# Kernel tuning notes

Hardware: AMD Instinct MI355X
Metric: run time of the kernel (lower is better)

Reference implementation:

```python
import jax, jax.numpy as jnp
import numpy as np

B, N, T, F = 8, 5000, 24, 10
H = 128
HEADS = 4
HORIZON = 6
E = 80000
NEG_SLOPE = 0.2


def setup_inputs() -> dict:
    key = jax.random.key(0)
    ks = jax.random.split(key, 24)
    s = 0.1
    inp = {
        'x': jax.random.normal(ks[0], (B, N, T, F), jnp.float32),
        'w_ih0': jax.random.normal(ks[1], (3 * H, F), jnp.float32) * s,
        'w_hh0': jax.random.normal(ks[2], (3 * H, H), jnp.float32) * s,
        'b_ih0': jax.random.normal(ks[3], (3 * H,), jnp.float32) * s,
        'b_hh0': jax.random.normal(ks[4], (3 * H,), jnp.float32) * s,
        'w_ih1': jax.random.normal(ks[5], (3 * H, H), jnp.float32) * s,
        'w_hh1': jax.random.normal(ks[6], (3 * H, H), jnp.float32) * s,
        'b_ih1': jax.random.normal(ks[7], (3 * H,), jnp.float32) * s,
        'b_hh1': jax.random.normal(ks[8], (3 * H,), jnp.float32) * s,
        'gat1_w': jax.random.normal(ks[9], (HEADS * H, H), jnp.float32) * s,
        'gat1_asrc': jax.random.normal(ks[10], (HEADS, H), jnp.float32) * s,
        'gat1_adst': jax.random.normal(ks[11], (HEADS, H), jnp.float32) * s,
        'gat1_b': jax.random.normal(ks[12], (H,), jnp.float32) * s,
        'gat2_w': jax.random.normal(ks[13], (HEADS * H, H), jnp.float32) * s,
        'gat2_asrc': jax.random.normal(ks[14], (HEADS, H), jnp.float32) * s,
        'gat2_adst': jax.random.normal(ks[15], (HEADS, H), jnp.float32) * s,
        'gat2_b': jax.random.normal(ks[16], (H,), jnp.float32) * s,
        'fc_w': jax.random.normal(ks[17], (HORIZON, H), jnp.float32) * s,
        'fc_b': jax.random.normal(ks[18], (HORIZON,), jnp.float32) * s,
        'edge_index': jax.random.randint(ks[19], (2, E), 0, N, jnp.int64),
    }
    return inp


def _gru_layer(xs, w_ih, w_hh, b_ih, b_hh):
    # xs: [BN, T, Fin] -> outputs [BN, T, H] (PyTorch GRU gate order r,z,n)
    gi = jnp.einsum('btf,gf->btg', xs, w_ih) + b_ih  # [BN, T, 3H]
    h0 = jnp.zeros((xs.shape[0], H), xs.dtype)

    def step(h, gi_t):
        gh = h @ w_hh.T + b_hh
        i_r, i_z, i_n = jnp.split(gi_t, 3, axis=-1)
        h_r, h_z, h_n = jnp.split(gh, 3, axis=-1)
        r = jax.nn.sigmoid(i_r + h_r)
        z = jax.nn.sigmoid(i_z + h_z)
        n = jnp.tanh(i_n + r * h_n)
        h_new = (1.0 - z) * n + z * h
        return h_new, h_new

    _, hs = jax.lax.scan(step, h0, jnp.swapaxes(gi, 0, 1))
    return jnp.swapaxes(hs, 0, 1)


def _gat(h, src, dst, W, a_src, a_dst, b, num_nodes):
    # PyG GATConv, heads=4, concat=False (mean), self-loops already in src/dst
    wh = (h @ W.T).reshape(num_nodes, HEADS, H)          # [BN, heads, H]
    alpha_s = jnp.sum(wh * a_src[None], axis=-1)          # [BN, heads]
    alpha_d = jnp.sum(wh * a_dst[None], axis=-1)
    e = jax.nn.leaky_relu(alpha_s[src] + alpha_d[dst], NEG_SLOPE)  # [Eb, heads]
    emax = jax.ops.segment_max(e, dst, num_segments=num_nodes)
    emax = jnp.where(jnp.isfinite(emax), emax, 0.0)
    ex = jnp.exp(e - emax[dst])
    denom = jax.ops.segment_sum(ex, dst, num_segments=num_nodes)
    alpha = ex / (denom[dst] + 1e-16)                     # segment softmax over incoming edges
    out = jax.ops.segment_sum(alpha[..., None] * wh[src], dst, num_segments=num_nodes)
    return out.mean(axis=1) + b


def _batched_edges(edge_index):
    offsets = (jnp.arange(B, dtype=edge_index.dtype) * N)[:, None]
    src = (edge_index[0][None, :] + offsets).reshape(-1)
    dst = (edge_index[1][None, :] + offsets).reshape(-1)
    loops = jnp.arange(B * N, dtype=edge_index.dtype)     # PyG add_self_loops=True
    return jnp.concatenate([src, loops]), jnp.concatenate([dst, loops])


def reference(x, w_ih0, w_hh0, b_ih0, b_hh0, w_ih1, w_hh1, b_ih1, b_hh1,
              gat1_w, gat1_asrc, gat1_adst, gat1_b,
              gat2_w, gat2_asrc, gat2_adst, gat2_b,
              fc_w, fc_b, edge_index):
    src, dst = _batched_edges(edge_index)
    xs = x.reshape(B * N, T, F)
    h1 = _gru_layer(xs, w_ih0, w_hh0, b_ih0, b_hh0)
    h2 = _gru_layer(h1, w_ih1, w_hh1, b_ih1, b_hh1)
    temporal = h2[:, -1, :]                               # [B*N, H]
    s = jax.nn.relu(_gat(temporal, src, dst, gat1_w, gat1_asrc, gat1_adst, gat1_b, B * N))
    s = jax.nn.relu(_gat(s, src, dst, gat2_w, gat2_asrc, gat2_adst, gat2_b, B * N))
    out = s @ fc_w.T + fc_b
    return out.reshape(B, N, HORIZON)
```

## Files before the change

### kernel.cpp

```cpp
#include <hip/hip_runtime.h>
#include <math.h>

#define T_STEPS 24
#define F_IN 10
#define HDIM 128
#define E_EDGES 80000
#define B_BATCH 8
#define N_NODES 5000
#define BN_TOTAL 40000
#define BE 640000
#define NE 680000

typedef __attribute__((ext_vector_type(8))) short s16x8;
typedef __attribute__((ext_vector_type(4))) short s16x4;
typedef __attribute__((ext_vector_type(4))) float fx4;
typedef __attribute__((ext_vector_type(2))) float fx2;
typedef __attribute__((ext_vector_type(4))) unsigned int ux4;
typedef __attribute__((ext_vector_type(2))) unsigned int ux2;

__device__ __forceinline__ float sigmoidf_(float v) { return 1.f / (1.f + __expf(-v)); }
__device__ __forceinline__ float tanhf_(float v) { float e = __expf(2.f * v); return 1.f - 2.f / (e + 1.f); }

__device__ __forceinline__ short f2b(float f) {
    unsigned u = __float_as_uint(f);
    unsigned r = (u + 0x7fffu + ((u >> 16) & 1u)) >> 16;
    return (short)r;
}
__device__ __forceinline__ unsigned int pkbf(float a, float b) {
    unsigned int r;
    asm("v_cvt_pk_bf16_f32 %0, %1, %2" : "=v"(r) : "v"(a), "v"(b));
    return r;
}

#define VMW0 asm volatile("s_waitcnt vmcnt(0)" ::: "memory")

__global__ void pack_w(const float* __restrict__ wih0, const float* __restrict__ whh0,
                       const float* __restrict__ wih1, const float* __restrict__ whh1,
                       const float* __restrict__ g1w, const float* __restrict__ g2w,
                       short* __restrict__ pk) {
    int id = blockIdx.x * 256 + threadIdx.x;
    if (id >= 290816) return;
    if (id < 147456) {
        int mat = id / 49152, r = id % 49152;
        int nf = r / 2048, r2 = r % 2048, kf = r2 / 512, r3 = r2 % 512, lane = r3 / 8, j = r3 % 8;
        int n = nf * 16 + (lane & 15), k = kf * 32 + (lane >> 4) * 8 + j;
        const float* src = (mat == 0) ? whh0 : (mat == 1) ? whh1 : wih1;
        pk[id] = f2b(src[n * 128 + k]);
    } else if (id < 159744) {
        int r = id - 147456;
        int nf = r / 512, r2 = r % 512, lane = r2 / 8, j = r2 % 8;
        int n = nf * 16 + (lane & 15), k = (lane >> 4) * 8 + j;
        pk[id] = (k < F_IN) ? f2b(wih0[n * F_IN + k]) : (short)0;
    } else {
        const float* src = (id < 225280) ? g1w : g2w;
        int r = (id < 225280) ? (id - 159744) : (id - 225280);
        int nf = r / 2048, r2 = r % 2048, kf = r2 / 512, r3 = r2 % 512, lane = r3 / 8, j = r3 % 8;
        int n = nf * 16 + (lane & 15), k = kf * 32 + (lane >> 4) * 8 + j;
        pk[id] = f2b(src[n * 128 + k]);
    }
}

__global__ __launch_bounds__(512, 1) void gru_mfma(
    const float* __restrict__ x, const short* __restrict__ pk,
    const float* __restrict__ bih0, const float* __restrict__ bhh0,
    const float* __restrict__ bih1, const float* __restrict__ bhh1,
    float* __restrict__ temporal) {
    __shared__ __align__(16) short h1b[64 * 128];
    __shared__ __align__(16) short h2b[64 * 128];
    __shared__ __align__(16) short ih1s[49152];
    __shared__ __align__(16) short ih0s[12288];
    __shared__ __align__(16) float blds[2][4][128];
    const int tid = threadIdx.x;
    const int w = tid >> 6, l = tid & 63;
    const int lm = l & 15, lk = l >> 4;
    const int jb = w * 16 + lk * 4;
    const long sb = (long)blockIdx.x * 64;

    {
        const char* src1 = (const char*)(pk + 98304);
#pragma unroll
        for (int r = 0; r < 12; ++r) {
            const int off = (w * 12 + r) * 1024;
            __builtin_amdgcn_global_load_lds(
                (const __attribute__((address_space(1))) unsigned int*)(src1 + off + l * 16),
                (__attribute__((address_space(3))) unsigned int*)((char*)ih1s + off), 16, 0, 0);
        }
        const char* src0 = (const char*)(pk + 147456);
#pragma unroll
        for (int r = 0; r < 3; ++r) {
            const int off = (w * 3 + r) * 1024;
            __builtin_amdgcn_global_load_lds(
                (const __attribute__((address_space(1))) unsigned int*)(src0 + off + l * 16),
                (__attribute__((address_space(3))) unsigned int*)((char*)ih0s + off), 16, 0, 0);
        }
    }
    if (tid < 128) {
        const int j = tid;
        blds[0][0][j] = bih0[j] + bhh0[j];
        blds[0][1][j] = bih0[128 + j] + bhh0[128 + j];
        blds[0][2][j] = bhh0[256 + j];
        blds[0][3][j] = bih0[256 + j];
    } else if (tid < 256) {
        const int j = tid - 128;
        blds[1][0][j] = bih1[j] + bhh1[j];
        blds[1][1][j] = bih1[128 + j] + bhh1[128 + j];
        blds[1][2][j] = bhh1[256 + j];
        blds[1][3][j] = bih1[256 + j];
    }
    for (int i = tid; i < 64 * 128; i += 512) { h1b[i] = 0; h2b[i] = 0; }

    s16x8 whh0r[3][4], whh1r[3][4];
#pragma unroll
    for (int g = 0; g < 3; ++g)
#pragma unroll
        for (int kf = 0; kf < 4; ++kf) {
            const int idx = ((((g * 8 + w) * 4) + kf) * 64 + l) * 8;
            whh0r[g][kf] = *(const s16x8*)&pk[idx];
            whh1r[g][kf] = *(const s16x8*)&pk[49152 + idx];
        }

    fx4 h1s[4], h2s[4];
#pragma unroll
    for (int mf = 0; mf < 4; ++mf) { h1s[mf] = (fx4)(0.f); h2s[mf] = (fx4)(0.f); }

    VMW0;
    __syncthreads();

    for (int tt = 0; tt < T_STEPS; ++tt) {
        ux4 xu[4];
#pragma unroll
        for (int mf = 0; mf < 4; ++mf) {
            fx2 a0 = (fx2)(0.f), a1 = (fx2)(0.f), a2 = (fx2)(0.f), a3 = (fx2)(0.f);
            const float* xr = x + (sb + mf * 16 + lm) * (T_STEPS * F_IN) + tt * F_IN;
            if (lk == 0) {
                a0 = *(const fx2*)(xr);     a1 = *(const fx2*)(xr + 2);
                a2 = *(const fx2*)(xr + 4); a3 = *(const fx2*)(xr + 6);
            } else if (lk == 1) {
                a0 = *(const fx2*)(xr + 8);
            }
            ux4 t = { pkbf(a0.x, a0.y), pkbf(a1.x, a1.y), pkbf(a2.x, a2.y), pkbf(a3.x, a3.y) };
            xu[mf] = t;
        }
        fx4 acc[4][4];
#pragma unroll
        for (int p = 0; p < 4; ++p) {
            const fx4 bv = *(const fx4*)&blds[0][p][jb];
#pragma unroll
            for (int mf = 0; mf < 4; ++mf) acc[p][mf] = bv;
        }
#pragma unroll
        for (int kf = 0; kf < 4; ++kf) {
            s16x8 bfr[4];
#pragma unroll
            for (int mf = 0; mf < 4; ++mf) {
                const int m = mf * 16 + lm;
                const int slot = (kf * 4 + lk) ^ (m & 7);
                bfr[mf] = *(const s16x8*)&h1b[m * 128 + slot * 8];
            }
#pragma unroll
            for (int g = 0; g < 3; ++g) {
                const int part = (g == 2) ? 2 : g;
#pragma unroll
                for (int mf = 0; mf < 4; ++mf)
                    acc[part][mf] = __builtin_amdgcn_mfma_f32_16x16x32_bf16(whh0r[g][kf], bfr[mf], acc[part][mf], 0, 0, 0);
            }
        }
#pragma unroll
        for (int g = 0; g < 3; ++g) {
            const int part = (g == 2) ? 3 : g;
            const s16x8 af = *(const s16x8*)&ih0s[((g * 8 + w) * 64 + l) * 8];
#pragma unroll
            for (int mf = 0; mf < 4; ++mf)
                acc[part][mf] = __builtin_amdgcn_mfma_f32_16x16x32_bf16(af, __builtin_bit_cast(s16x8, xu[mf]), acc[part][mf], 0, 0, 0);
        }
        ux2 w1[4];
#pragma unroll
        for (int mf = 0; mf < 4; ++mf) {
#pragma unroll
            for (int rg = 0; rg < 4; ++rg) {
                const float r = sigmoidf_(acc[0][mf][rg]);
                const float z = sigmoidf_(acc[1][mf][rg]);
                const float n = tanhf_(acc[3][mf][rg] + r * acc[2][mf][rg]);
                h1s[mf][rg] = (1.f - z) * n + z * h1s[mf][rg];
            }
            ux2 q = { pkbf(h1s[mf][0], h1s[mf][1]), pkbf(h1s[mf][2], h1s[mf][3]) };
            w1[mf] = q;
        }
#pragma unroll
        for (int p = 0; p < 4; ++p) {
            const fx4 bv = *(const fx4*)&blds[1][p][jb];
#pragma unroll
            for (int mf = 0; mf < 4; ++mf) acc[p][mf] = bv;
        }
#pragma unroll
        for (int kf = 0; kf < 4; ++kf) {
            s16x8 bfr[4];
#pragma unroll
            for (int mf = 0; mf < 4; ++mf) {
                const int m = mf * 16 + lm;
                const int slot = (kf * 4 + lk) ^ (m & 7);
                bfr[mf] = *(const s16x8*)&h2b[m * 128 + slot * 8];
            }
#pragma unroll
            for (int g = 0; g < 3; ++g) {
                const int part = (g == 2) ? 2 : g;
#pragma unroll
                for (int mf = 0; mf < 4; ++mf)
                    acc[part][mf] = __builtin_amdgcn_mfma_f32_16x16x32_bf16(whh1r[g][kf], bfr[mf], acc[part][mf], 0, 0, 0);
            }
        }
        __syncthreads();
#pragma unroll
        for (int mf = 0; mf < 4; ++mf) {
            const int m = mf * 16 + lm;
            const int slot = (jb >> 3) ^ (m & 7);
            *(ux2*)&h1b[m * 128 + slot * 8 + (jb & 7)] = w1[mf];
        }
        __syncthreads();
#pragma unroll
        for (int kf = 0; kf < 4; ++kf) {
            s16x8 bfr[4];
#pragma unroll
            for (int mf = 0; mf < 4; ++mf) {
                const int m = mf * 16 + lm;
                const int slot = (kf * 4 + lk) ^ (m & 7);
                bfr[mf] = *(const s16x8*)&h1b[m * 128 + slot * 8];
            }
#pragma unroll
            for (int g = 0; g < 3; ++g) {
                const int part = (g == 2) ? 3 : g;
                const s16x8 af = *(const s16x8*)&ih1s[((((g * 8 + w) * 4) + kf) * 64 + l) * 8];
#pragma unroll
                for (int mf = 0; mf < 4; ++mf)
                    acc[part][mf] = __builtin_amdgcn_mfma_f32_16x16x32_bf16(af, bfr[mf], acc[part][mf], 0, 0, 0);
            }
        }
#pragma unroll
        for (int mf = 0; mf < 4; ++mf) {
#pragma unroll
            for (int rg = 0; rg < 4; ++rg) {
                const float r = sigmoidf_(acc[0][mf][rg]);
                const float z = sigmoidf_(acc[1][mf][rg]);
                const float n = tanhf_(acc[3][mf][rg] + r * acc[2][mf][rg]);
                h2s[mf][rg] = (1.f - z) * n + z * h2s[mf][rg];
            }
            const int m = mf * 16 + lm;
            const int slot = (jb >> 3) ^ (m & 7);
            ux2 q = { pkbf(h2s[mf][0], h2s[mf][1]), pkbf(h2s[mf][2], h2s[mf][3]) };
            *(ux2*)&h2b[m * 128 + slot * 8 + (jb & 7)] = q;
        }
        __syncthreads();
    }
#pragma unroll
    for (int mf = 0; mf < 4; ++mf) {
        const long m = sb + mf * 16 + lm;
        *(fx4*)&temporal[m * 128 + jb] = h2s[mf];
    }
}

__global__ void csr_count(const int* __restrict__ edge1, int* __restrict__ cnt) {
    int e = blockIdx.x * 256 + threadIdx.x;
    if (e >= NE) return;
    int d;
    if (e < BE) { int b = e / E_EDGES; d = edge1[e - b * E_EDGES] + b * N_NODES; }
    else d = e - BE;
    atomicAdd(&cnt[d], 1);
}

__global__ void csr_scan(const int* cnt, int* offs, int* curs) {
    __shared__ int part[1024];
    const int t = threadIdx.x;
    const int base = t * 40;
    int end = base + 40; if (end > BN_TOTAL) end = BN_TOTAL;
    int s = 0;
    for (int i = base; i < end; ++i) s += cnt[i];
    part[t] = s;
    __syncthreads();
    for (int off = 1; off < 1024; off <<= 1) {
        int v = (t >= off) ? part[t - off] : 0;
        __syncthreads();
        part[t] += v;
        __syncthreads();
    }
    int run = part[t] - s;
    for (int i = base; i < end; ++i) {
        int c = cnt[i];
        offs[i] = run; curs[i] = run; run += c;
    }
    if (t == 1023) offs[BN_TOTAL] = NE;
}

__global__ void csr_fill(const int* __restrict__ edge1, int* __restrict__ curs, int* __restrict__ esort) {
    int e = blockIdx.x * 256 + threadIdx.x;
    if (e >= NE) return;
    int d;
    if (e < BE) { int b = e / E_EDGES; d = edge1[e - b * E_EDGES] + b * N_NODES; }
    else d = e - BE;
    int pos = atomicAdd(&curs[d], 1);
    esort[pos] = e;
}

__global__ __launch_bounds__(256, 2) void gat_gemm(const float* __restrict__ feat,
                                                   const short* __restrict__ pkg,
                                                   const float* __restrict__ asrc,
                                                   const float* __restrict__ adst,
                                                   float* __restrict__ wh,
                                                   float* __restrict__ AS, float* __restrict__ AD) {
    __shared__ __align__(16) short fb[128 * 128];
    __shared__ float reda[4][128];
    __shared__ float redb[4][128];
    const int tid = threadIdx.x;
    const int w = tid >> 6, l = tid & 63;
    const int lm = l & 15, lk = l >> 4;
    const int i0 = blockIdx.x * 128;
    const int j0 = blockIdx.y * 128;
#pragma unroll
    for (int it = 0; it < 16; ++it) {
        const int idx = it * 256 + tid;
        const int r = idx >> 5, kq = idx & 31;
        fx4 v = (fx4)(0.f);
        const int row = i0 + r;
        if (row < BN_TOTAL) v = *(const fx4*)&feat[(size_t)row * 128 + kq * 4];
        const int slot = (kq >> 1) ^ (r & 7);
        ux2 pv = { pkbf(v.x, v.y), pkbf(v.z, v.w) };
        *(ux2*)&fb[r * 128 + slot * 8 + (kq & 1) * 4] = pv;
    }
    __syncthreads();
    fx4 acc[2][8];
#pragma unroll
    for (int jf = 0; jf < 2; ++jf)
#pragma unroll
        for (int mf = 0; mf < 8; ++mf) acc[jf][mf] = (fx4)(0.f);
#pragma unroll
    for (int kf = 0; kf < 4; ++kf) {
        s16x8 bfr[8];
#pragma unroll
        for (int mf = 0; mf < 8; ++mf) {
            const int m = mf * 16 + lm;
            const int slot = (kf * 4 + lk) ^ (m & 7);
            bfr[mf] = *(const s16x8*)&fb[m * 128 + slot * 8];
        }
#pragma unroll
        for (int jf = 0; jf < 2; ++jf) {
            const int nf = (j0 >> 4) + w * 2 + jf;
            const s16x8 af = *(const s16x8*)&pkg[((nf * 4 + kf) * 64 + l) * 8];
#pragma unroll
            for (int mf = 0; mf < 8; ++mf)
                acc[jf][mf] = __builtin_amdgcn_mfma_f32_16x16x32_bf16(af, bfr[mf], acc[jf][mf], 0, 0, 0);
        }
    }
    float ps[8], pd[8];
#pragma unroll
    for (int mf = 0; mf < 8; ++mf) { ps[mf] = 0.f; pd[mf] = 0.f; }
#pragma unroll
    for (int jf = 0; jf < 2; ++jf) {
        const int cb = w * 32 + jf * 16 + lk * 4;
        const fx4 s4 = *(const fx4*)&asrc[j0 + cb];
        const fx4 d4 = *(const fx4*)&adst[j0 + cb];
        const int nb = j0 + cb;
#pragma unroll
        for (int mf = 0; mf < 8; ++mf) {
            const int m = i0 + mf * 16 + lm;
            const fx4 a = acc[jf][mf];
            if (m < BN_TOTAL) *(fx4*)&wh[(size_t)m * 512 + nb] = a;
            ps[mf] += a.x * s4.x + a.y * s4.y + a.z * s4.z + a.w * s4.w;
            pd[mf] += a.x * d4.x + a.y * d4.y + a.z * d4.z + a.w * d4.w;
        }
    }
#pragma unroll
    for (int off = 16; off <= 32; off <<= 1) {
#pragma unroll
        for (int mf = 0; mf < 8; ++mf) {
            ps[mf] += __shfl_xor(ps[mf], off);
            pd[mf] += __shfl_xor(pd[mf], off);
        }
    }
    if (lk == 0) {
#pragma unroll
        for (int mf = 0; mf < 8; ++mf) {
            reda[w][mf * 16 + lm] = ps[mf];
            redb[w][mf * 16 + lm] = pd[mf];
        }
    }
    __syncthreads();
    if (tid < 128) {
        const int row = i0 + tid;
        if (row < BN_TOTAL) {
            const float a = reda[0][tid] + reda[1][tid] + reda[2][tid] + reda[3][tid];
            const float b = redb[0][tid] + redb[1][tid] + redb[2][tid] + redb[3][tid];
            AS[row * 4 + (j0 >> 7)] = a;
            AD[row * 4 + (j0 >> 7)] = b;
        }
    }
}

__device__ __forceinline__ int decode_src(int eid, const int* __restrict__ edge0) {
    if (eid < BE) { int b = eid / E_EDGES; return edge0[eid - b * E_EDGES] + b * N_NODES; }
    return eid - BE;
}

__global__ __launch_bounds__(256) void gat_aggregate(const float* __restrict__ wh,
                                                     const float* __restrict__ AS, const float* __restrict__ AD,
                                                     const int* __restrict__ offs, const int* __restrict__ esort,
                                                     const int* __restrict__ edge0, const float* __restrict__ bias,
                                                     float* __restrict__ outf,
                                                     const float* __restrict__ fcw, const float* __restrict__ fcb,
                                                     float* __restrict__ out6) {
    const int lane = threadIdx.x & 63;
    const int bid = blockIdx.x;
    const int d = (bid & 7) * N_NODES + (bid >> 3) * 4 + (threadIdx.x >> 6);
    const int e0 = offs[d], e1 = offs[d + 1];
    const fx4 ad4 = *(const fx4*)&AD[d * 4];
    float mx0 = -1e30f, mx1 = -1e30f, mx2 = -1e30f, mx3 = -1e30f;
    float den0 = 0.f, den1 = 0.f, den2 = 0.f, den3 = 0.f;
    float acc[8] = {0.f, 0.f, 0.f, 0.f, 0.f, 0.f, 0.f, 0.f};
    for (int e = e0; e < e1; ++e) {
        const int src = decode_src(esort[e], edge0);
        const fx4 as4 = *(const fx4*)&AS[src * 4];
        float v0 = as4.x + ad4.x; v0 = v0 > 0.f ? v0 : 0.2f * v0;
        float v1 = as4.y + ad4.y; v1 = v1 > 0.f ? v1 : 0.2f * v1;
        float v2 = as4.z + ad4.z; v2 = v2 > 0.f ? v2 : 0.2f * v2;
        float v3 = as4.w + ad4.w; v3 = v3 > 0.f ? v3 : 0.2f * v3;
        const float n0 = fmaxf(mx0, v0), n1 = fmaxf(mx1, v1), n2 = fmaxf(mx2, v2), n3 = fmaxf(mx3, v3);
        const float c0 = __expf(mx0 - n0), c1 = __expf(mx1 - n1), c2 = __expf(mx2 - n2), c3 = __expf(mx3 - n3);
        const float ex0 = __expf(v0 - n0), ex1 = __expf(v1 - n1), ex2 = __expf(v2 - n2), ex3 = __expf(v3 - n3);
        mx0 = n0; mx1 = n1; mx2 = n2; mx3 = n3;
        den0 = den0 * c0 + ex0; den1 = den1 * c1 + ex1;
        den2 = den2 * c2 + ex2; den3 = den3 * c3 + ex3;
        const float* wr = wh + (size_t)src * 512;
        acc[0] = acc[0] * c0 + ex0 * wr[lane];        acc[1] = acc[1] * c0 + ex0 * wr[64 + lane];
        acc[2] = acc[2] * c1 + ex1 * wr[128 + lane];  acc[3] = acc[3] * c1 + ex1 * wr[192 + lane];
        acc[4] = acc[4] * c2 + ex2 * wr[256 + lane];  acc[5] = acc[5] * c2 + ex2 * wr[320 + lane];
        acc[6] = acc[6] * c3 + ex3 * wr[384 + lane];  acc[7] = acc[7] * c3 + ex3 * wr[448 + lane];
    }
    den0 += 1e-16f; den1 += 1e-16f; den2 += 1e-16f; den3 += 1e-16f;
    const float o0r = 0.25f * (acc[0] / den0 + acc[2] / den1 + acc[4] / den2 + acc[6] / den3) + bias[lane];
    const float o1r = 0.25f * (acc[1] / den0 + acc[3] / den1 + acc[5] / den2 + acc[7] / den3) + bias[64 + lane];
    const float o0 = fmaxf(o0r, 0.f);
    const float o1 = fmaxf(o1r, 0.f);
    if (fcw == nullptr) {
        outf[(size_t)d * 128 + lane] = o0;
        outf[(size_t)d * 128 + 64 + lane] = o1;
    } else {
        float p[6];
#pragma unroll
        for (int m = 0; m < 6; ++m) p[m] = o0 * fcw[m * 128 + lane] + o1 * fcw[m * 128 + 64 + lane];
#pragma unroll
        for (int off = 32; off > 0; off >>= 1) {
#pragma unroll
            for (int m = 0; m < 6; ++m) p[m] += __shfl_down(p[m], off);
        }
        if (lane == 0) {
#pragma unroll
            for (int m = 0; m < 6; ++m) out6[(size_t)d * 6 + m] = p[m] + fcb[m];
        }
    }
}

extern "C" void kernel_launch(void* const* d_in, const int* in_sizes, int n_in,
                              void* d_out, int out_size, void* d_ws, size_t ws_size,
                              hipStream_t stream) {
    const float* x = (const float*)d_in[0];
    const float* wih0 = (const float*)d_in[1];
    const float* whh0 = (const float*)d_in[2];
    const float* bih0 = (const float*)d_in[3];
    const float* bhh0 = (const float*)d_in[4];
    const float* wih1 = (const float*)d_in[5];
    const float* whh1 = (const float*)d_in[6];
    const float* bih1 = (const float*)d_in[7];
    const float* bhh1 = (const float*)d_in[8];
    const float* g1w = (const float*)d_in[9];
    const float* g1as = (const float*)d_in[10];
    const float* g1ad = (const float*)d_in[11];
    const float* g1b = (const float*)d_in[12];
    const float* g2w = (const float*)d_in[13];
    const float* g2as = (const float*)d_in[14];
    const float* g2ad = (const float*)d_in[15];
    const float* g2b = (const float*)d_in[16];
    const float* fcw = (const float*)d_in[17];
    const float* fcb = (const float*)d_in[18];
    const int* eidx = (const int*)d_in[19];
    const int* edge0 = eidx;
    const int* edge1 = eidx + E_EDGES;

    char* ws = (char*)d_ws;
    float* H0 = (float*)ws;
    float* H1 = (float*)(ws + 20480000);
    float* WH = (float*)(ws + 40960000);
    float* AS = (float*)(ws + 122880000);
    float* AD = (float*)(ws + 123520000);
    short* PK = (short*)(ws + 124160000);
    int* OFFS = (int*)(ws + 124765184);
    int* CURS = (int*)(ws + 124925248);
    int* ESORT = (int*)(ws + 125085248);

    hipMemsetAsync(CURS, 0, BN_TOTAL * sizeof(int), stream);
    pack_w<<<1136, 256, 0, stream>>>(wih0, whh0, wih1, whh1, g1w, g2w, PK);
    csr_count<<<(NE + 255) / 256, 256, 0, stream>>>(edge1, CURS);
    csr_scan<<<1, 1024, 0, stream>>>(CURS, OFFS, CURS);
    csr_fill<<<(NE + 255) / 256, 256, 0, stream>>>(edge1, CURS, ESORT);

    gru_mfma<<<625, 512, 0, stream>>>(x, PK, bih0, bhh0, bih1, bhh1, H0);

    dim3 gg(313, 4);
    gat_gemm<<<gg, 256, 0, stream>>>(H0, PK + 159744, g1as, g1ad, WH, AS, AD);
    gat_aggregate<<<10000, 256, 0, stream>>>(WH, AS, AD, OFFS, ESORT, edge0, g1b, H1,
                                             nullptr, nullptr, nullptr);

    gat_gemm<<<gg, 256, 0, stream>>>(H1, PK + 225280, g2as, g2ad, WH, AS, AD);
    gat_aggregate<<<10000, 256, 0, stream>>>(WH, AS, AD, OFFS, ESORT, edge0, g2b, nullptr,
                                             fcw, fcb, (float*)d_out);
}
```

Measured before the change: 1.304 ms.

## Keep GRU input weights in registers and store GAT projections as bf16

```diff
diff --git a/kernel.cpp b/kernel.cpp
--- a/kernel.cpp
+++ b/kernel.cpp
@@ -31,8 +31,9 @@
     asm("v_cvt_pk_bf16_f32 %0, %1, %2" : "=v"(r) : "v"(a), "v"(b));
     return r;
 }
-
-#define VMW0 asm volatile("s_waitcnt vmcnt(0)" ::: "memory")
+__device__ __forceinline__ float bfu(unsigned short u) {
+    return __uint_as_float(((unsigned)u) << 16);
+}
 
 __global__ void pack_w(const float* __restrict__ wih0, const float* __restrict__ whh0,
                        const float* __restrict__ wih1, const float* __restrict__ whh1,
@@ -67,8 +68,6 @@
     float* __restrict__ temporal) {
     __shared__ __align__(16) short h1b[64 * 128];
     __shared__ __align__(16) short h2b[64 * 128];
-    __shared__ __align__(16) short ih1s[49152];
-    __shared__ __align__(16) short ih0s[12288];
     __shared__ __align__(16) float blds[2][4][128];
     const int tid = threadIdx.x;
     const int w = tid >> 6, l = tid & 63;
@@ -76,24 +75,6 @@
     const int jb = w * 16 + lk * 4;
     const long sb = (long)blockIdx.x * 64;
 
-    {
-        const char* src1 = (const char*)(pk + 98304);
-#pragma unroll
-        for (int r = 0; r < 12; ++r) {
-            const int off = (w * 12 + r) * 1024;
-            __builtin_amdgcn_global_load_lds(
-                (const __attribute__((address_space(1))) unsigned int*)(src1 + off + l * 16),
-                (__attribute__((address_space(3))) unsigned int*)((char*)ih1s + off), 16, 0, 0);
-        }
-        const char* src0 = (const char*)(pk + 147456);
-#pragma unroll
-        for (int r = 0; r < 3; ++r) {
-            const int off = (w * 3 + r) * 1024;
-            __builtin_amdgcn_global_load_lds(
-                (const __attribute__((address_space(1))) unsigned int*)(src0 + off + l * 16),
-                (__attribute__((address_space(3))) unsigned int*)((char*)ih0s + off), 16, 0, 0);
-        }
-    }
     if (tid < 128) {
         const int j = tid;
         blds[0][0][j] = bih0[j] + bhh0[j];
@@ -109,21 +90,23 @@
     }
     for (int i = tid; i < 64 * 128; i += 512) { h1b[i] = 0; h2b[i] = 0; }
 
-    s16x8 whh0r[3][4], whh1r[3][4];
-#pragma unroll
-    for (int g = 0; g < 3; ++g)
+    s16x8 whh0r[3][4], whh1r[3][4], wih1r[3][4], wih0r[3];
+#pragma unroll
+    for (int g = 0; g < 3; ++g) {
 #pragma unroll
         for (int kf = 0; kf < 4; ++kf) {
             const int idx = ((((g * 8 + w) * 4) + kf) * 64 + l) * 8;
             whh0r[g][kf] = *(const s16x8*)&pk[idx];
             whh1r[g][kf] = *(const s16x8*)&pk[49152 + idx];
-        }
+            wih1r[g][kf] = *(const s16x8*)&pk[98304 + idx];
+        }
+        wih0r[g] = *(const s16x8*)&pk[147456 + ((g * 8 + w) * 64 + l) * 8];
+    }
 
     fx4 h1s[4], h2s[4];
 #pragma unroll
     for (int mf = 0; mf < 4; ++mf) { h1s[mf] = (fx4)(0.f); h2s[mf] = (fx4)(0.f); }
 
-    VMW0;
     __syncthreads();
 
     for (int tt = 0; tt < T_STEPS; ++tt) {
@@ -168,10 +151,9 @@
 #pragma unroll
         for (int g = 0; g < 3; ++g) {
             const int part = (g == 2) ? 3 : g;
-            const s16x8 af = *(const s16x8*)&ih0s[((g * 8 + w) * 64 + l) * 8];
 #pragma unroll
             for (int mf = 0; mf < 4; ++mf)
-                acc[part][mf] = __builtin_amdgcn_mfma_f32_16x16x32_bf16(af, __builtin_bit_cast(s16x8, xu[mf]), acc[part][mf], 0, 0, 0);
+                acc[part][mf] = __builtin_amdgcn_mfma_f32_16x16x32_bf16(wih0r[g], __builtin_bit_cast(s16x8, xu[mf]), acc[part][mf], 0, 0, 0);
         }
         ux2 w1[4];
 #pragma unroll
@@ -229,10 +211,9 @@
 #pragma unroll
             for (int g = 0; g < 3; ++g) {
                 const int part = (g == 2) ? 3 : g;
-                const s16x8 af = *(const s16x8*)&ih1s[((((g * 8 + w) * 4) + kf) * 64 + l) * 8];
 #pragma unroll
                 for (int mf = 0; mf < 4; ++mf)
-                    acc[part][mf] = __builtin_amdgcn_mfma_f32_16x16x32_bf16(af, bfr[mf], acc[part][mf], 0, 0, 0);
+                    acc[part][mf] = __builtin_amdgcn_mfma_f32_16x16x32_bf16(wih1r[g][kf], bfr[mf], acc[part][mf], 0, 0, 0);
             }
         }
 #pragma unroll
@@ -304,7 +285,7 @@
                                                    const short* __restrict__ pkg,
                                                    const float* __restrict__ asrc,
                                                    const float* __restrict__ adst,
-                                                   float* __restrict__ wh,
+                                                   unsigned short* __restrict__ whb,
                                                    float* __restrict__ AS, float* __restrict__ AD) {
     __shared__ __align__(16) short fb[128 * 128];
     __shared__ float reda[4][128];
@@ -362,7 +343,10 @@
         for (int mf = 0; mf < 8; ++mf) {
             const int m = i0 + mf * 16 + lm;
             const fx4 a = acc[jf][mf];
-            if (m < BN_TOTAL) *(fx4*)&wh[(size_t)m * 512 + nb] = a;
+            if (m < BN_TOTAL) {
+                ux2 pv = { pkbf(a.x, a.y), pkbf(a.z, a.w) };
+                *(ux2*)&whb[(size_t)m * 512 + nb] = pv;
+            }
             ps[mf] += a.x * s4.x + a.y * s4.y + a.z * s4.z + a.w * s4.w;
             pd[mf] += a.x * d4.x + a.y * d4.y + a.z * d4.z + a.w * d4.w;
         }
@@ -399,7 +383,7 @@
     return eid - BE;
 }
 
-__global__ __launch_bounds__(256) void gat_aggregate(const float* __restrict__ wh,
+__global__ __launch_bounds__(256) void gat_aggregate(const unsigned short* __restrict__ whb,
                                                      const float* __restrict__ AS, const float* __restrict__ AD,
                                                      const int* __restrict__ offs, const int* __restrict__ esort,
                                                      const int* __restrict__ edge0, const float* __restrict__ bias,
@@ -427,11 +411,11 @@
         mx0 = n0; mx1 = n1; mx2 = n2; mx3 = n3;
         den0 = den0 * c0 + ex0; den1 = den1 * c1 + ex1;
         den2 = den2 * c2 + ex2; den3 = den3 * c3 + ex3;
-        const float* wr = wh + (size_t)src * 512;
-        acc[0] = acc[0] * c0 + ex0 * wr[lane];        acc[1] = acc[1] * c0 + ex0 * wr[64 + lane];
-        acc[2] = acc[2] * c1 + ex1 * wr[128 + lane];  acc[3] = acc[3] * c1 + ex1 * wr[192 + lane];
-        acc[4] = acc[4] * c2 + ex2 * wr[256 + lane];  acc[5] = acc[5] * c2 + ex2 * wr[320 + lane];
-        acc[6] = acc[6] * c3 + ex3 * wr[384 + lane];  acc[7] = acc[7] * c3 + ex3 * wr[448 + lane];
+        const unsigned short* wr = whb + (size_t)src * 512;
+        acc[0] = acc[0] * c0 + ex0 * bfu(wr[lane]);        acc[1] = acc[1] * c0 + ex0 * bfu(wr[64 + lane]);
+        acc[2] = acc[2] * c1 + ex1 * bfu(wr[128 + lane]);  acc[3] = acc[3] * c1 + ex1 * bfu(wr[192 + lane]);
+        acc[4] = acc[4] * c2 + ex2 * bfu(wr[256 + lane]);  acc[5] = acc[5] * c2 + ex2 * bfu(wr[320 + lane]);
+        acc[6] = acc[6] * c3 + ex3 * bfu(wr[384 + lane]);  acc[7] = acc[7] * c3 + ex3 * bfu(wr[448 + lane]);
     }
     den0 += 1e-16f; den1 += 1e-16f; den2 += 1e-16f; den3 += 1e-16f;
     const float o0r = 0.25f * (acc[0] / den0 + acc[2] / den1 + acc[4] / den2 + acc[6] / den3) + bias[lane];
@@ -486,7 +470,7 @@
     char* ws = (char*)d_ws;
     float* H0 = (float*)ws;
     float* H1 = (float*)(ws + 20480000);
-    float* WH = (float*)(ws + 40960000);
+    unsigned short* WHB = (unsigned short*)(ws + 40960000);
     float* AS = (float*)(ws + 122880000);
     float* AD = (float*)(ws + 123520000);
     short* PK = (short*)(ws + 124160000);
@@ -503,11 +487,11 @@
     gru_mfma<<<625, 512, 0, stream>>>(x, PK, bih0, bhh0, bih1, bhh1, H0);
 
     dim3 gg(313, 4);
-    gat_gemm<<<gg, 256, 0, stream>>>(H0, PK + 159744, g1as, g1ad, WH, AS, AD);
-    gat_aggregate<<<10000, 256, 0, stream>>>(WH, AS, AD, OFFS, ESORT, edge0, g1b, H1,
+    gat_gemm<<<gg, 256, 0, stream>>>(H0, PK + 159744, g1as, g1ad, WHB, AS, AD);
+    gat_aggregate<<<10000, 256, 0, stream>>>(WHB, AS, AD, OFFS, ESORT, edge0, g1b, H1,
                                              nullptr, nullptr, nullptr);
 
-    gat_gemm<<<gg, 256, 0, stream>>>(H1, PK + 225280, g2as, g2ad, WH, AS, AD);
-    gat_aggregate<<<10000, 256, 0, stream>>>(WH, AS, AD, OFFS, ESORT, edge0, g2b, nullptr,
+    gat_gemm<<<gg, 256, 0, stream>>>(H1, PK + 225280, g2as, g2ad, WHB, AS, AD);
+    gat_aggregate<<<10000, 256, 0, stream>>>(WHB, AS, AD, OFFS, ESORT, edge0, g2b, nullptr,
                                              fcw, fcb, (float*)d_out);
 }
```

After: 1.393 ms. +6.8%, slower.

## Store GAT projected features as bf16 and use fast reciprocals in activations

Applied to the files above, without the earlier changes.

```diff
diff --git a/kernel.cpp b/kernel.cpp
--- a/kernel.cpp
+++ b/kernel.cpp
@@ -18,8 +18,9 @@
 typedef __attribute__((ext_vector_type(4))) unsigned int ux4;
 typedef __attribute__((ext_vector_type(2))) unsigned int ux2;
 
-__device__ __forceinline__ float sigmoidf_(float v) { return 1.f / (1.f + __expf(-v)); }
-__device__ __forceinline__ float tanhf_(float v) { float e = __expf(2.f * v); return 1.f - 2.f / (e + 1.f); }
+__device__ __forceinline__ float rcpf_(float v) { return __builtin_amdgcn_rcpf(v); }
+__device__ __forceinline__ float sigmoidf_(float v) { return rcpf_(1.f + __expf(-v)); }
+__device__ __forceinline__ float tanhf_(float v) { float e = __expf(2.f * v); return 1.f - 2.f * rcpf_(e + 1.f); }
 
 __device__ __forceinline__ short f2b(float f) {
     unsigned u = __float_as_uint(f);
@@ -30,6 +31,9 @@
     unsigned int r;
     asm("v_cvt_pk_bf16_f32 %0, %1, %2" : "=v"(r) : "v"(a), "v"(b));
     return r;
+}
+__device__ __forceinline__ float bfu(unsigned short u) {
+    return __uint_as_float(((unsigned)u) << 16);
 }
 
 #define VMW0 asm volatile("s_waitcnt vmcnt(0)" ::: "memory")
@@ -181,7 +185,7 @@
                 const float r = sigmoidf_(acc[0][mf][rg]);
                 const float z = sigmoidf_(acc[1][mf][rg]);
                 const float n = tanhf_(acc[3][mf][rg] + r * acc[2][mf][rg]);
-                h1s[mf][rg] = (1.f - z) * n + z * h1s[mf][rg];
+                h1s[mf][rg] = n + z * (h1s[mf][rg] - n);
             }
             ux2 q = { pkbf(h1s[mf][0], h1s[mf][1]), pkbf(h1s[mf][2], h1s[mf][3]) };
             w1[mf] = q;
@@ -242,7 +246,7 @@
                 const float r = sigmoidf_(acc[0][mf][rg]);
                 const float z = sigmoidf_(acc[1][mf][rg]);
                 const float n = tanhf_(acc[3][mf][rg] + r * acc[2][mf][rg]);
-                h2s[mf][rg] = (1.f - z) * n + z * h2s[mf][rg];
+                h2s[mf][rg] = n + z * (h2s[mf][rg] - n);
             }
             const int m = mf * 16 + lm;
             const int slot = (jb >> 3) ^ (m & 7);
@@ -304,7 +308,7 @@
                                                    const short* __restrict__ pkg,
                                                    const float* __restrict__ asrc,
                                                    const float* __restrict__ adst,
-                                                   float* __restrict__ wh,
+                                                   unsigned short* __restrict__ whb,
                                                    float* __restrict__ AS, float* __restrict__ AD) {
     __shared__ __align__(16) short fb[128 * 128];
     __shared__ float reda[4][128];
@@ -362,7 +366,10 @@
         for (int mf = 0; mf < 8; ++mf) {
             const int m = i0 + mf * 16 + lm;
             const fx4 a = acc[jf][mf];
-            if (m < BN_TOTAL) *(fx4*)&wh[(size_t)m * 512 + nb] = a;
+            if (m < BN_TOTAL) {
+                ux2 pv = { pkbf(a.x, a.y), pkbf(a.z, a.w) };
+                *(ux2*)&whb[(size_t)m * 512 + nb] = pv;
+            }
             ps[mf] += a.x * s4.x + a.y * s4.y + a.z * s4.z + a.w * s4.w;
             pd[mf] += a.x * d4.x + a.y * d4.y + a.z * d4.z + a.w * d4.w;
         }
@@ -399,7 +406,7 @@
     return eid - BE;
 }
 
-__global__ __launch_bounds__(256) void gat_aggregate(const float* __restrict__ wh,
+__global__ __launch_bounds__(256) void gat_aggregate(const unsigned short* __restrict__ whb,
                                                      const float* __restrict__ AS, const float* __restrict__ AD,
                                                      const int* __restrict__ offs, const int* __restrict__ esort,
                                                      const int* __restrict__ edge0, const float* __restrict__ bias,
@@ -427,24 +434,34 @@
         mx0 = n0; mx1 = n1; mx2 = n2; mx3 = n3;
         den0 = den0 * c0 + ex0; den1 = den1 * c1 + ex1;
         den2 = den2 * c2 + ex2; den3 = den3 * c3 + ex3;
-        const float* wr = wh + (size_t)src * 512;
-        acc[0] = acc[0] * c0 + ex0 * wr[lane];        acc[1] = acc[1] * c0 + ex0 * wr[64 + lane];
-        acc[2] = acc[2] * c1 + ex1 * wr[128 + lane];  acc[3] = acc[3] * c1 + ex1 * wr[192 + lane];
-        acc[4] = acc[4] * c2 + ex2 * wr[256 + lane];  acc[5] = acc[5] * c2 + ex2 * wr[320 + lane];
-        acc[6] = acc[6] * c3 + ex3 * wr[384 + lane];  acc[7] = acc[7] * c3 + ex3 * wr[448 + lane];
-    }
-    den0 += 1e-16f; den1 += 1e-16f; den2 += 1e-16f; den3 += 1e-16f;
-    const float o0r = 0.25f * (acc[0] / den0 + acc[2] / den1 + acc[4] / den2 + acc[6] / den3) + bias[lane];
-    const float o1r = 0.25f * (acc[1] / den0 + acc[3] / den1 + acc[5] / den2 + acc[7] / den3) + bias[64 + lane];
+        const unsigned int* wr = (const unsigned int*)(whb + (size_t)src * 512);
+        const unsigned int u0 = wr[lane];
+        const unsigned int u1 = wr[64 + lane];
+        const unsigned int u2 = wr[128 + lane];
+        const unsigned int u3 = wr[192 + lane];
+        acc[0] = acc[0] * c0 + ex0 * bfu((unsigned short)u0);
+        acc[1] = acc[1] * c0 + ex0 * bfu((unsigned short)(u0 >> 16));
+        acc[2] = acc[2] * c1 + ex1 * bfu((unsigned short)u1);
+        acc[3] = acc[3] * c1 + ex1 * bfu((unsigned short)(u1 >> 16));
+        acc[4] = acc[4] * c2 + ex2 * bfu((unsigned short)u2);
+        acc[5] = acc[5] * c2 + ex2 * bfu((unsigned short)(u2 >> 16));
+        acc[6] = acc[6] * c3 + ex3 * bfu((unsigned short)u3);
+        acc[7] = acc[7] * c3 + ex3 * bfu((unsigned short)(u3 >> 16));
+    }
+    const float i0v = rcpf_(den0 + 1e-16f), i1v = rcpf_(den1 + 1e-16f);
+    const float i2v = rcpf_(den2 + 1e-16f), i3v = rcpf_(den3 + 1e-16f);
+    const int c0i = 2 * lane, c1i = 2 * lane + 1;
+    const float o0r = 0.25f * (acc[0] * i0v + acc[2] * i1v + acc[4] * i2v + acc[6] * i3v) + bias[c0i];
+    const float o1r = 0.25f * (acc[1] * i0v + acc[3] * i1v + acc[5] * i2v + acc[7] * i3v) + bias[c1i];
     const float o0 = fmaxf(o0r, 0.f);
     const float o1 = fmaxf(o1r, 0.f);
     if (fcw == nullptr) {
-        outf[(size_t)d * 128 + lane] = o0;
-        outf[(size_t)d * 128 + 64 + lane] = o1;
+        fx2 ov = { o0, o1 };
+        *(fx2*)&outf[(size_t)d * 128 + c0i] = ov;
     } else {
         float p[6];
 #pragma unroll
-        for (int m = 0; m < 6; ++m) p[m] = o0 * fcw[m * 128 + lane] + o1 * fcw[m * 128 + 64 + lane];
+        for (int m = 0; m < 6; ++m) p[m] = o0 * fcw[m * 128 + c0i] + o1 * fcw[m * 128 + c1i];
 #pragma unroll
         for (int off = 32; off > 0; off >>= 1) {
 #pragma unroll
@@ -486,7 +503,7 @@
     char* ws = (char*)d_ws;
     float* H0 = (float*)ws;
     float* H1 = (float*)(ws + 20480000);
-    float* WH = (float*)(ws + 40960000);
+    unsigned short* WHB = (unsigned short*)(ws + 40960000);
     float* AS = (float*)(ws + 122880000);
     float* AD = (float*)(ws + 123520000);
     short* PK = (short*)(ws + 124160000);
@@ -503,11 +520,11 @@
     gru_mfma<<<625, 512, 0, stream>>>(x, PK, bih0, bhh0, bih1, bhh1, H0);
 
     dim3 gg(313, 4);
-    gat_gemm<<<gg, 256, 0, stream>>>(H0, PK + 159744, g1as, g1ad, WH, AS, AD);
-    gat_aggregate<<<10000, 256, 0, stream>>>(WH, AS, AD, OFFS, ESORT, edge0, g1b, H1,
+    gat_gemm<<<gg, 256, 0, stream>>>(H0, PK + 159744, g1as, g1ad, WHB, AS, AD);
+    gat_aggregate<<<10000, 256, 0, stream>>>(WHB, AS, AD, OFFS, ESORT, edge0, g1b, H1,
                                              nullptr, nullptr, nullptr);
 
-    gat_gemm<<<gg, 256, 0, stream>>>(H1, PK + 225280, g2as, g2ad, WH, AS, AD);
-    gat_aggregate<<<10000, 256, 0, stream>>>(WH, AS, AD, OFFS, ESORT, edge0, g2b, nullptr,
+    gat_gemm<<<gg, 256, 0, stream>>>(H1, PK + 225280, g2as, g2ad, WHB, AS, AD);
+    gat_aggregate<<<10000, 256, 0, stream>>>(WHB, AS, AD, OFFS, ESORT, edge0, g2b, nullptr,
                                              fcw, fcb, (float*)d_out);
 }
```

After: 1.047 ms. -19.7%, faster.
